# Performance work log

Hardware: AMD Instinct MI355X
Metric: run time of the kernel (lower is better)

## Reference

```python
import jax, jax.numpy as jnp
import numpy as np

N_ITEMS = 1_000_000
IN_DIM, HID_DIM, OUT_DIM = 64, 256, 128
N_BINS = 4096


def setup_inputs() -> dict:
    key = jax.random.key(0)
    k1, k2, k3, k4 = jax.random.split(key, 4)
    x = jax.random.normal(k1, (N_ITEMS, IN_DIM), dtype=jnp.float32)
    idxs = jax.random.randint(k2, (N_ITEMS,), 0, N_BINS, dtype=jnp.int64)
    W1 = jax.random.normal(k3, (IN_DIM, HID_DIM), dtype=jnp.float32) * (1.0 / np.sqrt(IN_DIM))
    b1 = jnp.zeros((HID_DIM,), dtype=jnp.float32)
    W2 = jax.random.normal(k4, (HID_DIM, OUT_DIM), dtype=jnp.float32) * (1.0 / np.sqrt(HID_DIM))
    b2 = jnp.zeros((OUT_DIM,), dtype=jnp.float32)
    return {"x": x, "idxs": idxs, "n_bins": N_BINS, "W1": W1, "b1": b1, "W2": W2, "b2": b2}


def reference(x, idxs, n_bins, W1, b1, W2, b2):
    # MLP: Linear -> ReLU -> Linear (per item)
    h = jax.nn.relu(x @ W1 + b1)            # [N, HID]
    items_encoded = h @ W2 + b2             # [N, OUT]
    # scatter-add into bins (torch.index_put_ with accumulate=True)
    embeddings = jax.ops.segment_sum(items_encoded, idxs, num_segments=n_bins)  # [n_bins, OUT]
    return embeddings
```

## Files before the change

### kernel.cpp

```cpp
#include <hip/hip_runtime.h>
#include <hip/hip_bf16.h>

typedef __attribute__((ext_vector_type(8))) short short8;
typedef __attribute__((ext_vector_type(4))) float f32x4;
typedef __attribute__((ext_vector_type(4))) int int4v;

#define CAPB  384
#define NSCAT 128
#define NBINS 4096

__device__ inline unsigned short f2bf(float f) {
  unsigned u = __float_as_uint(f);
  return (unsigned short)((u + 0x7FFFu + ((u >> 16) & 1u)) >> 16);
}
__device__ inline short bfc(float f) {
  __hip_bfloat16 h = __float2bfloat16(f);
  return *(short*)&h;
}
__device__ inline __attribute__((always_inline))
f32x4 mfma16(short8 a, short8 b, f32x4 c) {
  return __builtin_amdgcn_mfma_f32_16x16x32_bf16(a, b, c, 0, 0, 0);
}
__device__ __forceinline__ void gload_lds16(const void* g, void* l) {
  __builtin_amdgcn_global_load_lds(
      (const __attribute__((address_space(1))) void*)g,
      (__attribute__((address_space(3))) void*)l, 16, 0, 0);
}

__global__ __launch_bounds__(256)
void bin_hist(const int* __restrict__ idxs, int* __restrict__ wsCnt,
              int* __restrict__ wsOff, int n_items)
{
  __shared__ int hist[NBINS];
  const int tid = threadIdx.x;
  for (int b = tid; b < NBINS; b += 256) hist[b] = 0;
  __syncthreads();

  const int nq = n_items >> 2;
  const int chunk = (nq + NSCAT - 1) / NSCAT;
  const int s0 = blockIdx.x * chunk;
  const int s1 = min(nq, s0 + chunk);
  const int4v* idx4 = (const int4v*)idxs;
  for (int s = s0 + tid; s < s1; s += 256) {
    int4v v = idx4[s];
    atomicAdd(&hist[v[0]], 1);
    atomicAdd(&hist[v[1]], 1);
    atomicAdd(&hist[v[2]], 1);
    atomicAdd(&hist[v[3]], 1);
  }
  if (blockIdx.x == NSCAT - 1)
    for (int i = (nq << 2) + tid; i < n_items; i += 256)
      atomicAdd(&hist[idxs[i]], 1);
  __syncthreads();

  for (int b = tid; b < NBINS; b += 256) {
    int c = hist[b];
    if (c) wsOff[b * NSCAT + blockIdx.x] = atomicAdd(&wsCnt[b], c);
  }
}

__global__ __launch_bounds__(256)
void scatter_ids(const int* __restrict__ idxs, const int* __restrict__ wsOff,
                 int* __restrict__ wsIds, int n_items)
{
  __shared__ int cur[NBINS];
  const int tid = threadIdx.x;
  for (int b = tid; b < NBINS; b += 256) cur[b] = wsOff[b * NSCAT + blockIdx.x];
  __syncthreads();

  const int nq = n_items >> 2;
  const int chunk = (nq + NSCAT - 1) / NSCAT;
  const int s0 = blockIdx.x * chunk;
  const int s1 = min(nq, s0 + chunk);
  const int4v* idx4 = (const int4v*)idxs;
  for (int s = s0 + tid; s < s1; s += 256) {
    int4v v = idx4[s];
    #pragma unroll
    for (int e = 0; e < 4; ++e) {
      int b = v[e];
      int pos = atomicAdd(&cur[b], 1);
      if (pos < CAPB) wsIds[b * CAPB + pos] = s * 4 + e;
    }
  }
  if (blockIdx.x == NSCAT - 1)
    for (int i = (nq << 2) + tid; i < n_items; i += 256) {
      int b = idxs[i];
      int pos = atomicAdd(&cur[b], 1);
      if (pos < CAPB) wsIds[b * CAPB + pos] = i;
    }
}

#define LDS_BYTES 153344

__global__ __launch_bounds__(512)
void mlp_bin9(const float* __restrict__ x,
              const float* __restrict__ W1,
              const float* __restrict__ b1,
              const float* __restrict__ W2,
              const float* __restrict__ b2,
              const int* __restrict__ wsCnt,
              const int* __restrict__ wsIds,
              float* __restrict__ out)
{
  extern __shared__ char smem[];
  unsigned short* sW1 = (unsigned short*)smem;
  char*           sStage = smem + 32768;
  unsigned short* sW2 = (unsigned short*)(smem + 32768);
  float* sB1 = (float*)(smem + 131072);
  float* sB2 = (float*)(smem + 132096);
  unsigned short* sHs = (unsigned short*)(smem + 132608);
  int*   sIds = (int*)(smem + 141056);

  const int tid = threadIdx.x;
  const int myblk = blockIdx.x;

  for (int f = tid; f < 16384; f += 512) {
    int blk = f >> 9;
    int mt = blk >> 1, kt = blk & 1;
    int ln = (f >> 3) & 63, j = f & 7;
    int qq = ln >> 4, cc = ln & 15;
    sW1[f] = f2bf(W1[(32*kt + 8*qq + j)*256 + 16*mt + cc]);
  }
  if (tid < 256) sB1[tid] = b1[tid];
  if (tid < 128) sB2[tid] = b2[tid];
  __syncthreads();

  const int lane = tid & 63;
  const int wave = tid >> 6;
  const int c = lane & 15;
  const int q = lane >> 4;
  char* myStage = sStage + wave * 12288;
  int*  myIds   = sIds + wave * 384;

  auto issue = [&](int pp, int cnt) {
    char* dst = myStage + (pp % 3) * 4096;
    #pragma unroll
    for (int i = 0; i < 4; ++i) {
      int r = i*4 + (lane >> 4);
      int slot = pp*16 + r;
      int id = myIds[min(slot, cnt - 1)];
      int g = (lane & 15) ^ (r & 7);
      gload_lds16(x + (long)id * 64 + g * 4, dst + i * 1024);
    }
  };
  auto cvtrow = [&](const char* buf, bool valid, short8& o0, short8& o1) {
    f32x4 v00 = *(const f32x4*)(buf + c*256 + (((2*q + 0)) ^ (c & 7))*16);
    f32x4 v01 = *(const f32x4*)(buf + c*256 + (((2*q + 1)) ^ (c & 7))*16);
    f32x4 v10 = *(const f32x4*)(buf + c*256 + (((8 + 2*q + 0)) ^ (c & 7))*16);
    f32x4 v11 = *(const f32x4*)(buf + c*256 + (((8 + 2*q + 1)) ^ (c & 7))*16);
    short8 f0, f1;
    f0[0]=bfc(v00[0]); f0[1]=bfc(v00[1]); f0[2]=bfc(v00[2]); f0[3]=bfc(v00[3]);
    f0[4]=bfc(v01[0]); f0[5]=bfc(v01[1]); f0[6]=bfc(v01[2]); f0[7]=bfc(v01[3]);
    f1[0]=bfc(v10[0]); f1[1]=bfc(v10[1]); f1[2]=bfc(v10[2]); f1[3]=bfc(v10[3]);
    f1[4]=bfc(v11[0]); f1[5]=bfc(v11[1]); f1[6]=bfc(v11[2]); f1[7]=bfc(v11[3]);
    short8 z = {0,0,0,0,0,0,0,0};
    o0 = valid ? f0 : z;
    o1 = valid ? f1 : z;
  };

  #pragma unroll 1
  for (int bsel = 0; bsel < 2; ++bsel) {
    const int lb = wave * 2 + bsel;
    const int gbin = myblk * 16 + lb;
    const int cnt = min(wsCnt[gbin], CAPB);
    const int passes = (cnt + 15) >> 4;
    const int npass2 = ((passes + 1) >> 1) << 1;
    const int* idsG = wsIds + gbin * CAPB;

    for (int j = lane; j < cnt; j += 64) myIds[j] = idsG[j];
    asm volatile("s_waitcnt vmcnt(0)" ::: "memory");

    float hsum[8][8];
    #pragma unroll
    for (int a = 0; a < 8; ++a)
      #pragma unroll
      for (int bq = 0; bq < 8; ++bq) hsum[a][bq] = 0.f;

    if (npass2 > 0) {
      issue(0, cnt);
      issue(1, cnt);
      if (2 < npass2) issue(2, cnt);
    }

    for (int pp = 0; pp < npass2; pp += 2) {
      if (pp + 2 < npass2) {
        asm volatile("s_waitcnt vmcnt(4)" ::: "memory");
      } else {
        asm volatile("s_waitcnt vmcnt(0)" ::: "memory");
      }
      const char* bufA = myStage + ((pp    ) % 3) * 4096;
      const char* bufB = myStage + ((pp + 1) % 3) * 4096;

      short8 xfA[2], xfB[2];
      cvtrow(bufA, (pp*16 + c) < cnt, xfA[0], xfA[1]);
      cvtrow(bufB, ((pp+1)*16 + c) < cnt, xfB[0], xfB[1]);

      if (pp + 3 < npass2) issue(pp + 3, cnt);
      if (pp + 4 < npass2) issue(pp + 4, cnt);

      #pragma unroll
      for (int kt2 = 0; kt2 < 8; ++kt2) {
        #pragma unroll
        for (int half = 0; half < 2; ++half) {
          const int mt = 2*kt2 + half;
          f32x4 bias = *(const f32x4*)(sB1 + 16*mt + 4*q);
          f32x4 gA = bias, gB = bias;
          short8 w0 = *(const short8*)(sW1 + (mt*2 + 0)*512 + lane*8);
          gA = mfma16(w0, xfA[0], gA);
          gB = mfma16(w0, xfB[0], gB);
          short8 w1 = *(const short8*)(sW1 + (mt*2 + 1)*512 + lane*8);
          gA = mfma16(w1, xfA[1], gA);
          gB = mfma16(w1, xfB[1], gB);
          #pragma unroll
          for (int r = 0; r < 4; ++r)
            hsum[kt2][half*4 + r] += fmaxf(gA[r], 0.f) + fmaxf(gB[r], 0.f);
        }
      }
    }

    const int n_inv = npass2*16 - cnt;
    if (n_inv > 0) {
      const float fn = (float)n_inv;
      #pragma unroll
      for (int kt2 = 0; kt2 < 8; ++kt2)
        #pragma unroll
        for (int half = 0; half < 2; ++half)
          #pragma unroll
          for (int r = 0; r < 4; ++r)
            hsum[kt2][half*4 + r] -= fn * fmaxf(sB1[16*(2*kt2+half) + 4*q + r], 0.f);
    }

    #pragma unroll
    for (int a = 0; a < 8; ++a)
      #pragma unroll
      for (int bq = 0; bq < 8; ++bq) {
        float v = hsum[a][bq];
        v += __shfl_xor(v, 1);
        v += __shfl_xor(v, 2);
        v += __shfl_xor(v, 4);
        v += __shfl_xor(v, 8);
        hsum[a][bq] = v;
      }

    if (c == 0) {
      #pragma unroll
      for (int kt2 = 0; kt2 < 8; ++kt2)
        #pragma unroll
        for (int half = 0; half < 2; ++half) {
          unsigned d0 = (unsigned)f2bf(hsum[kt2][half*4+0]) | ((unsigned)f2bf(hsum[kt2][half*4+1]) << 16);
          unsigned d1 = (unsigned)f2bf(hsum[kt2][half*4+2]) | ((unsigned)f2bf(hsum[kt2][half*4+3]) << 16);
          unsigned* dst = (unsigned*)(sHs + lb*264 + kt2*32 + half*16 + 4*q);
          dst[0] = d0; dst[1] = d1;
        }
    }
  }
  __syncthreads();

  for (int f = tid; f < 32768; f += 512) {
    int blk = f >> 9;
    int mt2 = blk >> 3, kt2 = blk & 7;
    int ln = (f >> 3) & 63, j = f & 7;
    int qq = ln >> 4, cc = ln & 15;
    sW2[f] = f2bf(W2[(32*kt2 + 8*qq + j)*128 + 16*mt2 + cc]);
  }
  __syncthreads();

  {
    const int mt2 = wave;
    f32x4 acc = {0.f, 0.f, 0.f, 0.f};
    #pragma unroll
    for (int kt2 = 0; kt2 < 8; ++kt2) {
      short8 w2 = *(const short8*)(sW2 + (mt2*8 + kt2)*512 + lane*8);
      short8 hf = *(const short8*)(sHs + c*264 + kt2*32 + 8*q);
      acc = mfma16(w2, hf, acc);
    }
    const int cntc = min(wsCnt[myblk*16 + c], CAPB);
    f32x4 res;
    #pragma unroll
    for (int r = 0; r < 4; ++r)
      res[r] = acc[r] + (float)cntc * sB2[16*mt2 + 4*q + r];
    float* op = out + ((long)myblk*16 + c)*128 + 16*mt2 + 4*q;
    *(f32x4*)op = res;
  }
}

extern "C" void kernel_launch(void* const* d_in, const int* in_sizes, int n_in,
                              void* d_out, int out_size, void* d_ws, size_t ws_size,
                              hipStream_t stream) {
  const float* x  = (const float*)d_in[0];
  const int* idxs = (const int*)d_in[1];
  const float* W1 = (const float*)d_in[3];
  const float* b1 = (const float*)d_in[4];
  const float* W2 = (const float*)d_in[5];
  const float* b2 = (const float*)d_in[6];
  float* out = (float*)d_out;
  const int n_items = in_sizes[1];
  const int n_bins = out_size / 128;
  const int nblocks = n_bins / 16;

  int* wsCnt = (int*)d_ws;
  int* wsOff = wsCnt + NBINS;
  int* wsIds = wsOff + NBINS * NSCAT;

  hipMemsetAsync(wsCnt, 0, (size_t)n_bins * sizeof(int), stream);
  bin_hist<<<NSCAT, 256, 0, stream>>>(idxs, wsCnt, wsOff, n_items);
  scatter_ids<<<NSCAT, 256, 0, stream>>>(idxs, wsOff, wsIds, n_items);
  mlp_bin9<<<nblocks, 512, LDS_BYTES, stream>>>(x, W1, b1, W2, b2, wsCnt, wsIds, out);
}
```

Before: 123.7 us.

## Fuse histogram and scatter kernels into one prep_sort kernel

Merges the bin histogram and id-scatter passes into a single kernel that keeps each block's reserved per-bin offsets in LDS, so the wsOff round trip through global memory and one kernel launch go away. The scatter block count drops from 128 to 64, and the id writes use nontemporal stores. The trade-off is fewer blocks doing the serial counting work, which lowers parallelism in the prep stage. The order of items within a bin can also change, so the float summation order may differ.

```diff
diff --git a/kernel.cpp b/kernel.cpp
--- a/kernel.cpp
+++ b/kernel.cpp
@@ -6,7 +6,7 @@
 typedef __attribute__((ext_vector_type(4))) int int4v;
 
 #define CAPB  384
-#define NSCAT 128
+#define NSCAT 64
 #define NBINS 4096
 
 __device__ inline unsigned short f2bf(float f) {
@@ -28,8 +28,8 @@
 }
 
 __global__ __launch_bounds__(256)
-void bin_hist(const int* __restrict__ idxs, int* __restrict__ wsCnt,
-              int* __restrict__ wsOff, int n_items)
+void prep_sort(const int* __restrict__ idxs, int* __restrict__ wsCnt,
+               int* __restrict__ wsIds, int n_items)
 {
   __shared__ int hist[NBINS];
   const int tid = threadIdx.x;
@@ -41,6 +41,7 @@
   const int s0 = blockIdx.x * chunk;
   const int s1 = min(nq, s0 + chunk);
   const int4v* idx4 = (const int4v*)idxs;
+
   for (int s = s0 + tid; s < s1; s += 256) {
     int4v v = idx4[s];
     atomicAdd(&hist[v[0]], 1);
@@ -55,38 +56,24 @@
 
   for (int b = tid; b < NBINS; b += 256) {
     int c = hist[b];
-    if (c) wsOff[b * NSCAT + blockIdx.x] = atomicAdd(&wsCnt[b], c);
-  }
-}
-
-__global__ __launch_bounds__(256)
-void scatter_ids(const int* __restrict__ idxs, const int* __restrict__ wsOff,
-                 int* __restrict__ wsIds, int n_items)
-{
-  __shared__ int cur[NBINS];
-  const int tid = threadIdx.x;
-  for (int b = tid; b < NBINS; b += 256) cur[b] = wsOff[b * NSCAT + blockIdx.x];
-  __syncthreads();
-
-  const int nq = n_items >> 2;
-  const int chunk = (nq + NSCAT - 1) / NSCAT;
-  const int s0 = blockIdx.x * chunk;
-  const int s1 = min(nq, s0 + chunk);
-  const int4v* idx4 = (const int4v*)idxs;
+    if (c) hist[b] = atomicAdd(&wsCnt[b], c);
+  }
+  __syncthreads();
+
   for (int s = s0 + tid; s < s1; s += 256) {
     int4v v = idx4[s];
     #pragma unroll
     for (int e = 0; e < 4; ++e) {
       int b = v[e];
-      int pos = atomicAdd(&cur[b], 1);
-      if (pos < CAPB) wsIds[b * CAPB + pos] = s * 4 + e;
+      int pos = atomicAdd(&hist[b], 1);
+      if (pos < CAPB) __builtin_nontemporal_store(s * 4 + e, &wsIds[b * CAPB + pos]);
     }
   }
   if (blockIdx.x == NSCAT - 1)
     for (int i = (nq << 2) + tid; i < n_items; i += 256) {
       int b = idxs[i];
-      int pos = atomicAdd(&cur[b], 1);
-      if (pos < CAPB) wsIds[b * CAPB + pos] = i;
+      int pos = atomicAdd(&hist[b], 1);
+      if (pos < CAPB) __builtin_nontemporal_store(i, &wsIds[b * CAPB + pos]);
     }
 }
 
@@ -299,11 +286,9 @@
   const int nblocks = n_bins / 16;
 
   int* wsCnt = (int*)d_ws;
-  int* wsOff = wsCnt + NBINS;
-  int* wsIds = wsOff + NBINS * NSCAT;
+  int* wsIds = wsCnt + NBINS;
 
   hipMemsetAsync(wsCnt, 0, (size_t)n_bins * sizeof(int), stream);
-  bin_hist<<<NSCAT, 256, 0, stream>>>(idxs, wsCnt, wsOff, n_items);
-  scatter_ids<<<NSCAT, 256, 0, stream>>>(idxs, wsOff, wsIds, n_items);
+  prep_sort<<<NSCAT, 256, 0, stream>>>(idxs, wsCnt, wsIds, n_items);
   mlp_bin9<<<nblocks, 512, LDS_BYTES, stream>>>(x, W1, b1, W2, b2, wsCnt, wsIds, out);
 }
```

Result: slower. 135.4 us (+9.4%).

## Process three staged passes per iteration with batched prefetch of next three

Applied to the files above, without the earlier changes.

Restructures the per-bin inner loop to convert and compute three 16-item passes per iteration instead of two. All three staging buffers are consumed, then the next three loads are issued before the MFMA work. This amortizes waits and feeds more independent MFMAs per weight load. The cost is a full vmcnt(0) drain each iteration instead of keeping a load in flight, and padding to a multiple of three passes, which adds wasted work.

```diff
diff --git a/kernel.cpp b/kernel.cpp
--- a/kernel.cpp
+++ b/kernel.cpp
@@ -93,14 +93,14 @@
 #define LDS_BYTES 153344
 
 __global__ __launch_bounds__(512)
-void mlp_bin9(const float* __restrict__ x,
-              const float* __restrict__ W1,
-              const float* __restrict__ b1,
-              const float* __restrict__ W2,
-              const float* __restrict__ b2,
-              const int* __restrict__ wsCnt,
-              const int* __restrict__ wsIds,
-              float* __restrict__ out)
+void mlp_bin10(const float* __restrict__ x,
+               const float* __restrict__ W1,
+               const float* __restrict__ b1,
+               const float* __restrict__ W2,
+               const float* __restrict__ b2,
+               const int* __restrict__ wsCnt,
+               const int* __restrict__ wsIds,
+               float* __restrict__ out)
 {
   extern __shared__ char smem[];
   unsigned short* sW1 = (unsigned short*)smem;
@@ -164,7 +164,7 @@
     const int gbin = myblk * 16 + lb;
     const int cnt = min(wsCnt[gbin], CAPB);
     const int passes = (cnt + 15) >> 4;
-    const int npass2 = ((passes + 1) >> 1) << 1;
+    const int npass = ((passes + 2) / 3) * 3;
     const int* idsG = wsIds + gbin * CAPB;
 
     for (int j = lane; j < cnt; j += 64) myIds[j] = idsG[j];
@@ -176,27 +176,25 @@
       #pragma unroll
       for (int bq = 0; bq < 8; ++bq) hsum[a][bq] = 0.f;
 
-    if (npass2 > 0) {
-      issue(0, cnt);
-      issue(1, cnt);
-      if (2 < npass2) issue(2, cnt);
-    }
-
-    for (int pp = 0; pp < npass2; pp += 2) {
-      if (pp + 2 < npass2) {
-        asm volatile("s_waitcnt vmcnt(4)" ::: "memory");
-      } else {
-        asm volatile("s_waitcnt vmcnt(0)" ::: "memory");
-      }
-      const char* bufA = myStage + ((pp    ) % 3) * 4096;
-      const char* bufB = myStage + ((pp + 1) % 3) * 4096;
-
-      short8 xfA[2], xfB[2];
+    if (npass > 0) { issue(0, cnt); issue(1, cnt); issue(2, cnt); }
+
+    for (int pp = 0; pp < npass; pp += 3) {
+      asm volatile("s_waitcnt vmcnt(0)" ::: "memory");
+      const char* bufA = myStage;
+      const char* bufB = myStage + 4096;
+      const char* bufC = myStage + 8192;
+
+      short8 xfA[2], xfB[2], xfC[2];
       cvtrow(bufA, (pp*16 + c) < cnt, xfA[0], xfA[1]);
       cvtrow(bufB, ((pp+1)*16 + c) < cnt, xfB[0], xfB[1]);
-
-      if (pp + 3 < npass2) issue(pp + 3, cnt);
-      if (pp + 4 < npass2) issue(pp + 4, cnt);
+      cvtrow(bufC, ((pp+2)*16 + c) < cnt, xfC[0], xfC[1]);
+      asm volatile("s_waitcnt lgkmcnt(0)" ::: "memory");
+
+      if (pp + 3 < npass) {
+        issue(pp + 3, cnt);
+        if (pp + 4 < npass) issue(pp + 4, cnt);
+        if (pp + 5 < npass) issue(pp + 5, cnt);
+      }
 
       #pragma unroll
       for (int kt2 = 0; kt2 < 8; ++kt2) {
@@ -204,21 +202,23 @@
         for (int half = 0; half < 2; ++half) {
           const int mt = 2*kt2 + half;
           f32x4 bias = *(const f32x4*)(sB1 + 16*mt + 4*q);
-          f32x4 gA = bias, gB = bias;
+          f32x4 gA = bias, gB = bias, gC = bias;
           short8 w0 = *(const short8*)(sW1 + (mt*2 + 0)*512 + lane*8);
           gA = mfma16(w0, xfA[0], gA);
           gB = mfma16(w0, xfB[0], gB);
+          gC = mfma16(w0, xfC[0], gC);
           short8 w1 = *(const short8*)(sW1 + (mt*2 + 1)*512 + lane*8);
           gA = mfma16(w1, xfA[1], gA);
           gB = mfma16(w1, xfB[1], gB);
+          gC = mfma16(w1, xfC[1], gC);
           #pragma unroll
           for (int r = 0; r < 4; ++r)
-            hsum[kt2][half*4 + r] += fmaxf(gA[r], 0.f) + fmaxf(gB[r], 0.f);
+            hsum[kt2][half*4 + r] += fmaxf(gA[r], 0.f) + fmaxf(gB[r], 0.f) + fmaxf(gC[r], 0.f);
         }
       }
     }
 
-    const int n_inv = npass2*16 - cnt;
+    const int n_inv = npass*16 - cnt;
     if (n_inv > 0) {
       const float fn = (float)n_inv;
       #pragma unroll
@@ -305,5 +305,5 @@
   hipMemsetAsync(wsCnt, 0, (size_t)n_bins * sizeof(int), stream);
   bin_hist<<<NSCAT, 256, 0, stream>>>(idxs, wsCnt, wsOff, n_items);
   scatter_ids<<<NSCAT, 256, 0, stream>>>(idxs, wsOff, wsIds, n_items);
-  mlp_bin9<<<nblocks, 512, LDS_BYTES, stream>>>(x, W1, b1, W2, b2, wsCnt, wsIds, out);
-}
+  mlp_bin10<<<nblocks, 512, LDS_BYTES, stream>>>(x, W1, b1, W2, b2, wsCnt, wsIds, out);
+}
```

After: 122.4 us. Within noise of the previous version (-1.0%).
